# Kernel tuning notes

Hardware: AMD Instinct MI355X
Metric: run time of the kernel (lower is better)

The kernel has to match this reference:

```python
import jax, jax.numpy as jnp
from jax import lax
import numpy as np

NBITS = 3  # PartialSumLSQ bit width


def binarize(x):
    # straight-through sign (Binarize in BNN code modifies .data -> identity STE)
    return x + lax.stop_gradient(jnp.sign(x) - x)


def lsq(y, alpha):
    # LSQ quantizer for partial sums: q = round(clamp(y/a, Qn, Qp)) * a, STE round,
    # gradient-scaled step size (forward value unaffected by g).
    Qn, Qp = -(2 ** (NBITS - 1)), 2 ** (NBITS - 1) - 1
    g = 1.0 / np.sqrt(y.size * Qp)
    a = alpha * g + lax.stop_gradient(alpha - alpha * g)
    yc = jnp.clip(y / a, Qn, Qp)
    yq = yc + lax.stop_gradient(jnp.round(yc) - yc)
    return yq * a


def split_slices(xp, cgroups):
    # xp: [B, 128*cgroups, H+2, W+2]; reproduces split_tensor_128/256/512 ordering:
    # channel group outermost, then col offset j, then row offset i.
    H, W = xp.shape[2] - 2, xp.shape[3] - 2
    sl = [xp[:, g * 128:(g + 1) * 128, i:i + H, j:j + W]
          for g in range(cgroups) for j in range(3) for i in range(3)]
    return jnp.stack(sl)  # [S, B, 128, H, W]


def psum_stage(x, w, b, alpha, cgroups):
    # emulated 3x3 binary conv: pad, split into S shifted 128-ch slices, per-slice
    # binarized 1x1 conv + bias, LSQ-quantize each partial sum, accumulate.
    xp = jnp.pad(binarize(x), ((0, 0), (0, 0), (1, 1), (1, 1)))
    xs = split_slices(xp, cgroups)                      # [S,B,128,H,W]
    y = jnp.einsum('sbchw,soc->sbohw', xs, binarize(w)) + b[:, None, :, None, None]
    return jax.vmap(lsq)(y, alpha).sum(0)               # [B,Cout,H,W]


def maxpool2(x):
    return lax.reduce_window(x, -jnp.inf, lax.max, (1, 1, 2, 2), (1, 1, 2, 2), 'VALID')


def bn(x, g, b):
    # eval-mode BatchNorm with running_mean=0, running_var=1 -> affine
    s = (1, -1) + (1,) * (x.ndim - 2)
    return x * g.reshape(s) + b.reshape(s)


def htanh(x):
    return jnp.clip(x, -1.0, 1.0)


def _forward(x, conv1_w, conv1_b, s2_w, s2_b, s2_a, s3_w, s3_b, s3_a,
             s4_w, s4_b, s4_a, s5_w, s5_b, s5_a, s6_w, s6_b, s6_a,
             bn1_g, bn1_b, bn2_g, bn2_b, bn3_g, bn3_b, bn4_g, bn4_b,
             bn5_g, bn5_b, bn6_g, bn6_b, fc1_w, fc1_b, fc2_w, fc2_b,
             fc3_w, fc3_b, fbn1_g, fbn1_b, fbn2_g, fbn2_b, fbn3_g, fbn3_b):
    # conv1: 3->128 3x3 pad1; input has 3 channels -> not binarized, weight binarized
    h = lax.conv_general_dilated(x, binarize(conv1_w), (1, 1), ((1, 1), (1, 1)),
                                 dimension_numbers=('NCHW', 'OIHW', 'NCHW'))
    h = h + conv1_b[None, :, None, None]
    h = htanh(bn(h, bn1_g, bn1_b))
    h = psum_stage(h, s2_w, s2_b, s2_a, 1)   # 128->128, 9 slices, 32x32
    h = maxpool2(h)                          # 16x16
    h = htanh(bn(h, bn2_g, bn2_b))
    h = psum_stage(h, s3_w, s3_b, s3_a, 1)   # 128->256, 9 slices
    h = htanh(bn(h, bn3_g, bn3_b))
    h = psum_stage(h, s4_w, s4_b, s4_a, 2)   # 256->256, 18 slices
    h = maxpool2(h)                          # 8x8
    h = htanh(bn(h, bn4_g, bn4_b))
    h = psum_stage(h, s5_w, s5_b, s5_a, 2)   # 256->512, 18 slices
    h = htanh(bn(h, bn5_g, bn5_b))
    h = psum_stage(h, s6_w, s6_b, s6_a, 4)   # 512->512, 36 slices
    h = maxpool2(h)                          # 4x4
    h = htanh(bn(h, bn6_g, bn6_b))
    # binarized classifier: 512*4*4 -> 1024 -> 1024 -> num_classes
    f = binarize(h.reshape(h.shape[0], -1))
    f = f @ binarize(fc1_w).T + fc1_b
    f = htanh(f * fbn1_g + fbn1_b)
    f = binarize(f) @ binarize(fc2_w).T + fc2_b
    f = htanh(f * fbn2_g + fbn2_b)
    f = binarize(f) @ binarize(fc3_w).T + fc3_b
    return f * fbn3_g + fbn3_b


def setup_inputs() -> dict:
    key = jax.random.key(0)
    ks = iter(jax.random.split(key, 80))
    def rn(shape, scale=1.0):
        return jax.random.normal(next(ks), shape, jnp.float32) * scale
    d = {}
    d['x'] = rn((64, 3, 32, 32))
    d['conv1_w'] = rn((128, 3, 3, 3), 0.1)
    d['conv1_b'] = rn((128,), 0.01)
    stages = {'s2': (9, 128), 's3': (9, 256), 's4': (18, 256),
              's5': (18, 512), 's6': (36, 512)}
    for name, (S, co) in stages.items():
        d[name + '_w'] = rn((S, co, 128), 0.1)
        d[name + '_b'] = rn((S, co), 0.01)
        d[name + '_a'] = jax.random.uniform(next(ks), (S,), jnp.float32, 0.05, 0.15)
    for i, c in zip(range(1, 7), [128, 128, 256, 256, 512, 512]):
        d[f'bn{i}_g'] = jnp.ones((c,), jnp.float32) + rn((c,), 0.01)
        d[f'bn{i}_b'] = rn((c,), 0.01)
    d['fc1_w'] = rn((1024, 512 * 16), 0.02); d['fc1_b'] = rn((1024,), 0.01)
    d['fc2_w'] = rn((1024, 1024), 0.02);     d['fc2_b'] = rn((1024,), 0.01)
    d['fc3_w'] = rn((10, 1024), 0.02);       d['fc3_b'] = rn((10,), 0.01)
    for i, c in zip(range(1, 4), [1024, 1024, 10]):
        d[f'fbn{i}_g'] = jnp.ones((c,), jnp.float32) + rn((c,), 0.01)
        d[f'fbn{i}_b'] = rn((c,), 0.01)
    return d


def reference(x, conv1_w, conv1_b, s2_w, s2_b, s2_a, s3_w, s3_b, s3_a,
              s4_w, s4_b, s4_a, s5_w, s5_b, s5_a, s6_w, s6_b, s6_a,
              bn1_g, bn1_b, bn2_g, bn2_b, bn3_g, bn3_b, bn4_g, bn4_b,
              bn5_g, bn5_b, bn6_g, bn6_b, fc1_w, fc1_b, fc2_w, fc2_b,
              fc3_w, fc3_b, fbn1_g, fbn1_b, fbn2_g, fbn2_b, fbn3_g, fbn3_b):
    return _forward(x, conv1_w, conv1_b, s2_w, s2_b, s2_a, s3_w, s3_b, s3_a,
                    s4_w, s4_b, s4_a, s5_w, s5_b, s5_a, s6_w, s6_b, s6_a,
                    bn1_g, bn1_b, bn2_g, bn2_b, bn3_g, bn3_b, bn4_g, bn4_b,
                    bn5_g, bn5_b, bn6_g, bn6_b, fc1_w, fc1_b, fc2_w, fc2_b,
                    fc3_w, fc3_b, fbn1_g, fbn1_b, fbn2_g, fbn2_b, fbn3_g, fbn3_b)
```

## Files before the change

### kernel.cpp

```cpp
#include <hip/hip_runtime.h>
#include <hip/hip_bf16.h>

typedef unsigned long long u64;

struct PackArgs {
    const float* w[7];
    u64* out[7];
    int cnt[7];
    int total;
};

__global__ void k_packall(PackArgs A) {
    int gid = blockIdx.x * blockDim.x + threadIdx.x;
    int wid = gid >> 6;
    int lane = threadIdx.x & 63;
    if (wid >= A.total) return;
    int seg = 0, base = 0, pre = 0;
#pragma unroll
    for (int t = 0; t < 7; ++t) {
        if (wid >= pre) { seg = t; base = pre; }
        pre += A.cnt[t];
    }
    int li = wid - base;
    const float* p = A.w[seg] + ((size_t)li << 6);
    u64 m = __ballot(p[lane] > 0.f);
    if (lane == 0) A.out[seg][li] = m;
}

__global__ void k_packw_fc1(const float* __restrict__ w, u64* __restrict__ outT) {
    int gid = blockIdx.x * blockDim.x + threadIdx.x;
    int wid = gid >> 6;
    int lane = threadIdx.x & 63;
    if (wid >= 1024 * 8) return;
    int row = wid >> 3, gk = wid & 7;
    int g = gk >> 1, k = gk & 1;
    int c = g * 128 + k * 64 + lane;
    const float* p = w + (size_t)row * 8192 + (size_t)c * 16;
    float arr[16];
#pragma unroll
    for (int q = 0; q < 4; ++q) {
        float4 f = ((const float4*)p)[q];
        arr[4 * q + 0] = f.x; arr[4 * q + 1] = f.y;
        arr[4 * q + 2] = f.z; arr[4 * q + 3] = f.w;
    }
#pragma unroll
    for (int h = 0; h < 4; ++h)
#pragma unroll
    for (int xq = 0; xq < 4; ++xq) {
        u64 m = __ballot(arr[h * 4 + xq] > 0.f);
        if (lane == 0) {
            int wd = g * 32 + h * 8 + xq * 2 + k;
            outT[(size_t)wd * 1024 + row] = m;
        }
    }
}

struct LutArgs {
    const float* alpha[5];
    const float* bias[5];
    int off[5];
    int Cout[5];
    double ysize[5];
    int total;
};

__global__ void k_lutall(LutArgs A, double* __restrict__ lut2) {
    int idx = blockIdx.x * blockDim.x + threadIdx.x;
    if (idx >= A.total) return;
    int seg = 0;
#pragma unroll
    for (int t = 1; t < 5; ++t) if (idx >= A.off[t]) seg = t;
    int li = idx - A.off[seg];
    int s = li / A.Cout[seg];
    double gq = 1.0 / sqrt(A.ysize[seg] * 3.0);
    double al = (double)A.alpha[seg][s];
    double tg = al * gq;
    double a  = tg + (al - tg);
    double b  = (double)A.bias[seg][li];
    double q0 = rint(fmin(fmax(b / a, -4.0), 3.0));
    double qp = rint(fmin(fmax((2.0 + b) / a, -4.0), 3.0));
    double qn = rint(fmin(fmax((-2.0 + b) / a, -4.0), 3.0));
    double cz = q0 * a;
    lut2[(size_t)idx * 2 + 0] = qp * a - cz;
    lut2[(size_t)idx * 2 + 1] = qn * a - cz;
}

struct CzArgs {
    const float* alpha[5];
    const float* bias[5];
    int off[5];
    int S[5];
    int Cout[5];
    double ysize[5];
    int total;
};

__global__ void k_cz(CzArgs A, double* __restrict__ czv) {
    int idx = blockIdx.x * blockDim.x + threadIdx.x;
    if (idx >= A.total) return;
    int seg = 0;
#pragma unroll
    for (int t = 1; t < 5; ++t) if (idx >= A.off[t]) seg = t;
    int o = idx - A.off[seg];
    double gq = 1.0 / sqrt(A.ysize[seg] * 3.0);
    double CZ = 0.0;
    for (int s = 0; s < A.S[seg]; ++s) {
        double al = (double)A.alpha[seg][s];
        double tg = al * gq;
        double a  = tg + (al - tg);
        double b  = (double)A.bias[seg][s * A.Cout[seg] + o];
        double q0 = rint(fmin(fmax(b / a, -4.0), 3.0));
        CZ += q0 * a;
    }
    czv[idx] = CZ;
}

__global__ __launch_bounds__(128)
void k_conv1(const float* __restrict__ x, const float* __restrict__ w,
             const float* __restrict__ cb, const float* __restrict__ g1,
             const float* __restrict__ b1, u64* __restrict__ apack) {
    __shared__ double xs[3][3][34];
    int h = blockIdx.x & 31;
    int b = blockIdx.x >> 5;
    int tid = threadIdx.x;
    for (int idx = tid; idx < 306; idx += 128) {
        int dyy = idx / 102;
        int rem = idx - dyy * 102;
        int ci = rem / 34;
        int col = rem - ci * 34;
        int y = h + dyy - 1, xx = col - 1;
        double v = 0.0;
        if ((unsigned)y < 32u && (unsigned)xx < 32u)
            v = (double)x[((b * 3 + ci) * 32 + y) * 32 + xx];
        xs[dyy][ci][col] = v;
    }
    __syncthreads();
    int o = tid;
    double sg[3][3][3];
#pragma unroll
    for (int ci = 0; ci < 3; ++ci)
#pragma unroll
    for (int ky = 0; ky < 3; ++ky)
#pragma unroll
    for (int kx = 0; kx < 3; ++kx) {
        float wv = w[o * 27 + (ci * 3 + ky) * 3 + kx];
        sg[kx][ci][ky] = wv > 0.f ? 1.0 : (wv < 0.f ? -1.0 : 0.0);
    }
    double cbv = (double)cb[o], g1v = (double)g1[o], b1v = (double)b1[o];
    double A0 = 0.0, A1 = 0.0, A2 = 0.0;
    for (int pc = 0; pc < 34; ++pc) {
        double v[3][3];
#pragma unroll
        for (int ky = 0; ky < 3; ++ky)
#pragma unroll
        for (int ci = 0; ci < 3; ++ci)
            v[ky][ci] = xs[ky][ci][pc];
        A2 = 0.0;
#pragma unroll
        for (int ci = 0; ci < 3; ++ci)
#pragma unroll
        for (int ky = 0; ky < 3; ++ky) {
            A0 += v[ky][ci] * sg[2][ci][ky];
            A1 += v[ky][ci] * sg[1][ci][ky];
            A2 += v[ky][ci] * sg[0][ci][ky];
        }
        if (pc >= 2) {
            int wc = pc - 2;
            double t = (A0 + cbv) * g1v + b1v;
            u64 m = __ballot(t > 0.0);
            if ((tid & 63) == 0)
                apack[((size_t)(b * 1024 + h * 32 + wc)) * 2 + (tid >> 6)] = m;
        }
        A0 = A1; A1 = A2;
    }
}

template <int POOL, int G, int H, int W, int Cout, int OCHUNK, int NC>
__global__ __launch_bounds__(POOL * OCHUNK)
void k_stage(const u64* __restrict__ apack, const u64* __restrict__ wpack,
             const double* __restrict__ lut2, const double* __restrict__ czv,
             const float* __restrict__ gam, const float* __restrict__ bet,
             u64* __restrict__ opack) {
    constexpr int CW = W / NC;
    constexpr int Ho = H / POOL, Wo = W / POOL;
    constexpr int NOC = Cout / OCHUNK;
    constexpr int NROW = POOL + 2;
    constexpr int NCOL = CW + 2;
    constexpr int NT = POOL * OCHUNK;
    __shared__ alignas(16) u64 sact[G][NROW][NCOL][2];
    constexpr int PLP = (POOL == 2) ? 2 : 1;
    constexpr int PLO = (POOL == 2) ? OCHUNK : 1;
    constexpr int PLC = (POOL == 2) ? (CW / 2) : 1;
    __shared__ double pl[PLP][PLO][PLC];

    int bi = blockIdx.x;
    int oc = bi % NOC; bi /= NOC;
    int ch = bi % NC;  bi /= NC;
    int ph = bi % Ho;
    int b  = bi / Ho;
    int tid = threadIdx.x;
    int dy = tid / OCHUNK;
    int ol = tid - dy * OCHUNK;
    int o  = oc * OCHUNK + ol;
    int c0 = ch * CW;
    int ybase = ph * POOL - 1;

    constexpr int NWD = G * NROW * NCOL;
    for (int t = tid; t < NWD; t += NT) {
        int g = t / (NROW * NCOL);
        int rr = t - g * (NROW * NCOL);
        int yy = rr / NCOL;
        int xx = rr - yy * NCOL;
        int y = ybase + yy, x = c0 - 1 + xx;
        u64 v0 = 0, v1 = 0;
        if ((unsigned)y < (unsigned)H && (unsigned)x < (unsigned)W) {
            const u64* p = apack + (((size_t)((b * G + g) * H + y)) * W + x) * 2;
            v0 = p[0]; v1 = p[1];
        }
        sact[g][yy][xx][0] = v0;
        sact[g][yy][xx][1] = v1;
    }
    __syncthreads();

    double CZ = czv[o];
    double acc[CW];
#pragma unroll
    for (int c = 0; c < CW; ++c) acc[c] = CZ;

#pragma unroll
    for (int g = 0; g < G; ++g) {
#pragma unroll
        for (int j = 0; j < 3; ++j) {
#pragma unroll
            for (int i = 0; i < 3; ++i) {
                int s = g * 9 + j * 3 + i;
                int y = ph * POOL + dy + i - 1;
                if ((unsigned)y >= (unsigned)H) continue;
                size_t so = (size_t)s * Cout + o;
                u64 w0 = wpack[so * 2], w1 = wpack[so * 2 + 1];
                double dp = lut2[so * 2], dn = lut2[so * 2 + 1];
                bool cutlo = (ch == 0) && (j == 0);
                bool cuthi = (ch == NC - 1) && (j == 2);
                int yy = dy + i;
#pragma unroll
                for (int c = 0; c < CW; ++c) {
                    if ((c == 0 && cutlo) || (c == CW - 1 && cuthi)) continue;
                    u64 a0 = sact[g][yy][c + j][0];
                    u64 a1 = sact[g][yy][c + j][1];
                    int d = __popcll(a0 ^ w0) + __popcll(a1 ^ w1);
                    double val = (d < 64) ? dp : dn;
                    val = (d == 64) ? 0.0 : val;
                    acc[c] += val;
                }
            }
        }
    }

    double gv = (double)gam[o], bv = (double)bet[o];
    if constexpr (POOL == 1) {
#pragma unroll
        for (int c = 0; c < CW; ++c) {
            double t = acc[c] * gv + bv;
            u64 bm = __ballot(t > 0.0);
            if ((tid & 63) == 0) {
                int pw = c0 + c;
                opack[(((size_t)(b * (Cout >> 7) + (o >> 7)) * Ho + ph) * Wo + pw) * 2
                      + ((o >> 6) & 1)] = bm;
            }
        }
    } else {
#pragma unroll
        for (int c2 = 0; c2 < CW / 2; ++c2)
            pl[dy][ol][c2] = fmax(acc[2 * c2], acc[2 * c2 + 1]);
        __syncthreads();
        if (dy == 0) {
#pragma unroll
            for (int c2 = 0; c2 < CW / 2; ++c2) {
                double m = fmax(pl[0][ol][c2], pl[1][ol][c2]);
                double t = m * gv + bv;
                u64 bm = __ballot(t > 0.0);
                if ((tid & 63) == 0) {
                    int pw = c0 / 2 + c2;
                    opack[(((size_t)(b * (Cout >> 7) + (o >> 7)) * Ho + ph) * Wo + pw) * 2
                          + ((o >> 6) & 1)] = bm;
                }
            }
        }
    }
}

__global__ void k_fc_pack(const u64* __restrict__ apack, const u64* __restrict__ wpack,
                          int rstride, int wstride,
                          const float* __restrict__ bias, const float* __restrict__ gam,
                          const float* __restrict__ bet, u64* __restrict__ opack,
                          int nw, int Rwords) {
    int wg = blockIdx.x % Rwords;
    int b = blockIdx.x / Rwords;
    int r = wg * 64 + threadIdx.x;
    const u64* a = apack + (size_t)b * nw;
    const u64* wp = wpack + (size_t)r * rstride;
    int d = 0;
    for (int i = 0; i < nw; ++i) d += __popcll(a[i] ^ wp[(size_t)i * wstride]);
    double isum = (double)(nw * 64 - 2 * d);
    double t = (isum + (double)bias[r]) * (double)gam[r] + (double)bet[r];
    u64 m = __ballot(t > 0.0);
    if (threadIdx.x == 0) opack[(size_t)b * Rwords + wg] = m;
}

__global__ void k_fc3(const u64* __restrict__ apack, const u64* __restrict__ wpack,
                      const float* __restrict__ bias, const float* __restrict__ gam,
                      const float* __restrict__ bet, float* __restrict__ out) {
    int idx = blockIdx.x * blockDim.x + threadIdx.x;
    if (idx >= 640) return;
    int b = idx / 10, r = idx % 10;
    const u64* a = apack + (size_t)b * 16;
    const u64* wp = wpack + (size_t)r * 16;
    int d = 0;
    for (int i = 0; i < 16; ++i) d += __popcll(a[i] ^ wp[i]);
    double isum = (double)(1024 - 2 * d);
    out[idx] = (float)((isum + (double)bias[r]) * (double)gam[r] + (double)bet[r]);
}


extern "C" void kernel_launch(void* const* d_in, const int* in_sizes, int n_in,
                              void* d_out, int out_size, void* d_ws, size_t ws_size,
                              hipStream_t stream) {
    const float* x       = (const float*)d_in[0];
    const float* conv1_w = (const float*)d_in[1];
    const float* conv1_b = (const float*)d_in[2];
    const float* s_w[5]  = {(const float*)d_in[3], (const float*)d_in[6], (const float*)d_in[9],
                            (const float*)d_in[12], (const float*)d_in[15]};
    const float* s_b[5]  = {(const float*)d_in[4], (const float*)d_in[7], (const float*)d_in[10],
                            (const float*)d_in[13], (const float*)d_in[16]};
    const float* s_a[5]  = {(const float*)d_in[5], (const float*)d_in[8], (const float*)d_in[11],
                            (const float*)d_in[14], (const float*)d_in[17]};
    const float* bn_g[6], *bn_b[6];
    for (int i = 0; i < 6; ++i) { bn_g[i] = (const float*)d_in[18 + 2 * i]; bn_b[i] = (const float*)d_in[19 + 2 * i]; }
    const float* fc1_w = (const float*)d_in[30]; const float* fc1_b = (const float*)d_in[31];
    const float* fc2_w = (const float*)d_in[32]; const float* fc2_b = (const float*)d_in[33];
    const float* fc3_w = (const float*)d_in[34]; const float* fc3_b = (const float*)d_in[35];
    const float* fbn_g[3], *fbn_b[3];
    for (int i = 0; i < 3; ++i) { fbn_g[i] = (const float*)d_in[36 + 2 * i]; fbn_b[i] = (const float*)d_in[37 + 2 * i]; }

    size_t off = 0;
    auto alloc = [&](size_t bytes) { off = (off + 255) & ~(size_t)255; size_t o = off; off += bytes; return o; };
    char* ws = (char*)d_ws;
    size_t o_apA = alloc(1048576);
    size_t o_apB = alloc(1048576);
    size_t o_wp  = alloc((size_t)71424 * 8);
    size_t o_lut = alloc((size_t)35712 * 2 * 8);
    size_t o_cz  = alloc((size_t)1664 * 8);
    size_t o_wf1 = alloc((size_t)1024 * 128 * 8);
    size_t o_wf2 = alloc((size_t)1024 * 16 * 8);
    size_t o_wf3 = alloc((size_t)10 * 16 * 8 + 256);
    size_t o_fp1 = alloc((size_t)64 * 16 * 8);
    size_t o_fp2 = alloc((size_t)64 * 16 * 8);
    if (off > ws_size) return;

    u64* apA = (u64*)(ws + o_apA);
    u64* apB = (u64*)(ws + o_apB);
    u64* wpbuf = (u64*)(ws + o_wp);
    double* lut2 = (double*)(ws + o_lut);
    double* czbuf = (double*)(ws + o_cz);
    u64* wf1T = (u64*)(ws + o_wf1);
    u64* wf2 = (u64*)(ws + o_wf2);
    u64* wf3 = (u64*)(ws + o_wf3);
    u64* fp1 = (u64*)(ws + o_fp1);
    u64* fp2 = (u64*)(ws + o_fp2);

    const int rowoff[5] = {0, 1152, 3456, 8064, 17280};
    const int czoff[5]  = {0, 128, 384, 640, 1152};
    u64* wp[5];  double* lt[5];  double* cz[5];
    for (int i = 0; i < 5; ++i) {
        wp[i] = wpbuf + (size_t)rowoff[i] * 2;
        lt[i] = lut2 + (size_t)rowoff[i] * 2;
        cz[i] = czbuf + czoff[i];
    }

    PackArgs PA;
    const int scnt[5] = {2304, 4608, 9216, 18432, 36864};
    int tot = 0;
    for (int i = 0; i < 5; ++i) { PA.w[i] = s_w[i]; PA.out[i] = wp[i]; PA.cnt[i] = scnt[i]; tot += scnt[i]; }
    PA.w[5] = fc2_w; PA.out[5] = wf2; PA.cnt[5] = 1024 * 16; tot += 1024 * 16;
    PA.w[6] = fc3_w; PA.out[6] = wf3; PA.cnt[6] = 160;       tot += 160;
    PA.total = tot;
    {
        long long thr = (long long)tot * 64;
        k_packall<<<(int)((thr + 255) / 256), 256, 0, stream>>>(PA);
    }
    k_packw_fc1<<<(1024 * 8 * 64) / 256, 256, 0, stream>>>(fc1_w, wf1T);

    LutArgs LA;
    const int sS[5]    = {9, 9, 18, 18, 36};
    const int sCout[5] = {128, 256, 256, 512, 512};
    const double sYsz[5] = {8388608.0, 4194304.0, 4194304.0, 2097152.0, 2097152.0};
    for (int i = 0; i < 5; ++i) {
        LA.alpha[i] = s_a[i]; LA.bias[i] = s_b[i];
        LA.off[i] = rowoff[i]; LA.Cout[i] = sCout[i]; LA.ysize[i] = sYsz[i];
    }
    LA.total = 35712;
    k_lutall<<<(35712 + 255) / 256, 256, 0, stream>>>(LA, lut2);

    CzArgs CA;
    for (int i = 0; i < 5; ++i) {
        CA.alpha[i] = s_a[i]; CA.bias[i] = s_b[i];
        CA.off[i] = czoff[i]; CA.S[i] = sS[i]; CA.Cout[i] = sCout[i]; CA.ysize[i] = sYsz[i];
    }
    CA.total = 1664;
    k_cz<<<(1664 + 255) / 256, 256, 0, stream>>>(CA, czbuf);

    k_conv1<<<64 * 32, 128, 0, stream>>>(x, conv1_w, conv1_b, bn_g[0], bn_b[0], apA);

    k_stage<2, 1, 32, 32, 128, 128, 2><<<64 * 16 * 2, 256, 0, stream>>>(
        apA, wp[0], lt[0], cz[0], bn_g[1], bn_b[1], apB);
    k_stage<1, 1, 16, 16, 256, 256, 2><<<64 * 16 * 2, 256, 0, stream>>>(
        apB, wp[1], lt[1], cz[1], bn_g[2], bn_b[2], apA);
    k_stage<2, 2, 16, 16, 256, 256, 2><<<64 * 8 * 2, 512, 0, stream>>>(
        apA, wp[2], lt[2], cz[2], bn_g[3], bn_b[3], apB);
    k_stage<1, 2, 8, 8, 512, 512, 2><<<64 * 8 * 2, 512, 0, stream>>>(
        apB, wp[3], lt[3], cz[3], bn_g[4], bn_b[4], apA);
    k_stage<2, 4, 8, 8, 512, 256, 2><<<64 * 4 * 2 * 2, 512, 0, stream>>>(
        apA, wp[4], lt[4], cz[4], bn_g[5], bn_b[5], apB);

    k_fc_pack<<<64 * 16, 64, 0, stream>>>(apB, wf1T, 1, 1024, fc1_b, fbn_g[0], fbn_b[0], fp1, 128, 16);
    k_fc_pack<<<64 * 16, 64, 0, stream>>>(fp1, wf2, 16, 1, fc2_b, fbn_g[1], fbn_b[1], fp2, 16, 16);
    k_fc3<<<10, 64, 0, stream>>>(fp2, wf3, fc3_b, fbn_g[2], fbn_b[2], (float*)d_out);
}
```

Measured before the change: 237.3 us.

## Fuse prep and FC kernels, interleave weight/LUT, and restructure stage tiling for in-register pooling

Merges the four weight-packing and LUT/cz precompute kernels into one k_prep launch and the three FC kernels into a single per-batch k_fc_all kernel that keeps intermediate bits in shared memory. Interleaves packed weights with their two LUT doubles in one 4-word record so each slice needs one contiguous load. Reworks k_stage so each thread owns all pooling rows and several output columns, which lets max-pooling happen in registers without the shared pool buffer and extra barrier, and changes per-stage grid/thread shapes. This cuts launch count and sync overhead but raises register pressure per thread, and the FC kernel runs only 64 blocks.

```diff
diff --git a/kernel.cpp b/kernel.cpp
--- a/kernel.cpp
+++ b/kernel.cpp
@@ -1,118 +1,108 @@
 #include <hip/hip_runtime.h>
 #include <hip/hip_bf16.h>
+#include <math.h>
 
 typedef unsigned long long u64;
 
-struct PackArgs {
+struct PrepArgs {
     const float* w[7];
     u64* out[7];
     int cnt[7];
-    int total;
-};
-
-__global__ void k_packall(PackArgs A) {
-    int gid = blockIdx.x * blockDim.x + threadIdx.x;
-    int wid = gid >> 6;
-    int lane = threadIdx.x & 63;
-    if (wid >= A.total) return;
-    int seg = 0, base = 0, pre = 0;
-#pragma unroll
-    for (int t = 0; t < 7; ++t) {
-        if (wid >= pre) { seg = t; base = pre; }
-        pre += A.cnt[t];
-    }
-    int li = wid - base;
-    const float* p = A.w[seg] + ((size_t)li << 6);
-    u64 m = __ballot(p[lane] > 0.f);
-    if (lane == 0) A.out[seg][li] = m;
-}
-
-__global__ void k_packw_fc1(const float* __restrict__ w, u64* __restrict__ outT) {
-    int gid = blockIdx.x * blockDim.x + threadIdx.x;
-    int wid = gid >> 6;
-    int lane = threadIdx.x & 63;
-    if (wid >= 1024 * 8) return;
-    int row = wid >> 3, gk = wid & 7;
-    int g = gk >> 1, k = gk & 1;
-    int c = g * 128 + k * 64 + lane;
-    const float* p = w + (size_t)row * 8192 + (size_t)c * 16;
-    float arr[16];
-#pragma unroll
-    for (int q = 0; q < 4; ++q) {
-        float4 f = ((const float4*)p)[q];
-        arr[4 * q + 0] = f.x; arr[4 * q + 1] = f.y;
-        arr[4 * q + 2] = f.z; arr[4 * q + 3] = f.w;
-    }
-#pragma unroll
-    for (int h = 0; h < 4; ++h)
-#pragma unroll
-    for (int xq = 0; xq < 4; ++xq) {
-        u64 m = __ballot(arr[h * 4 + xq] > 0.f);
-        if (lane == 0) {
-            int wd = g * 32 + h * 8 + xq * 2 + k;
-            outT[(size_t)wd * 1024 + row] = m;
-        }
-    }
-}
-
-struct LutArgs {
+    int mode[7];
+    const float* fc1w;
+    u64* fc1T;
     const float* alpha[5];
     const float* bias[5];
-    int off[5];
-    int Cout[5];
-    double ysize[5];
-    int total;
+    int loff[5];
+    int lCout[5];
+    double gq[5];
+    u64* wlut;
+    double* czv;
+    int czoff[5];
+    int czS[5];
+    int R1, R2, R3, R4;
 };
 
-__global__ void k_lutall(LutArgs A, double* __restrict__ lut2) {
-    int idx = blockIdx.x * blockDim.x + threadIdx.x;
-    if (idx >= A.total) return;
-    int seg = 0;
-#pragma unroll
-    for (int t = 1; t < 5; ++t) if (idx >= A.off[t]) seg = t;
-    int li = idx - A.off[seg];
-    int s = li / A.Cout[seg];
-    double gq = 1.0 / sqrt(A.ysize[seg] * 3.0);
-    double al = (double)A.alpha[seg][s];
-    double tg = al * gq;
-    double a  = tg + (al - tg);
-    double b  = (double)A.bias[seg][li];
-    double q0 = rint(fmin(fmax(b / a, -4.0), 3.0));
-    double qp = rint(fmin(fmax((2.0 + b) / a, -4.0), 3.0));
-    double qn = rint(fmin(fmax((-2.0 + b) / a, -4.0), 3.0));
-    double cz = q0 * a;
-    lut2[(size_t)idx * 2 + 0] = qp * a - cz;
-    lut2[(size_t)idx * 2 + 1] = qn * a - cz;
-}
-
-struct CzArgs {
-    const float* alpha[5];
-    const float* bias[5];
-    int off[5];
-    int S[5];
-    int Cout[5];
-    double ysize[5];
-    int total;
-};
-
-__global__ void k_cz(CzArgs A, double* __restrict__ czv) {
-    int idx = blockIdx.x * blockDim.x + threadIdx.x;
-    if (idx >= A.total) return;
-    int seg = 0;
-#pragma unroll
-    for (int t = 1; t < 5; ++t) if (idx >= A.off[t]) seg = t;
-    int o = idx - A.off[seg];
-    double gq = 1.0 / sqrt(A.ysize[seg] * 3.0);
-    double CZ = 0.0;
-    for (int s = 0; s < A.S[seg]; ++s) {
+__global__ __launch_bounds__(256)
+void k_prep(PrepArgs A) {
+    int gid = blockIdx.x * 256 + threadIdx.x;
+    int lane = threadIdx.x & 63;
+    if (gid < A.R1) {
+        int wid = gid >> 6;
+        int seg = 0, base = 0, pre = 0;
+#pragma unroll
+        for (int t = 0; t < 7; ++t) {
+            if (wid >= pre) { seg = t; base = pre; }
+            pre += A.cnt[t];
+        }
+        int li = wid - base;
+        const float* p = A.w[seg] + ((size_t)li << 6);
+        u64 m = __ballot(p[lane] > 0.f);
+        if (lane == 0) {
+            int mode = A.mode[seg];
+            size_t idx = (mode == 1) ? ((size_t)(li >> 1) * 4 + (li & 1))
+                       : (mode == 2) ? ((size_t)(li & 15) * 1024 + (li >> 4))
+                       : (size_t)li;
+            A.out[seg][idx] = m;
+        }
+    } else if (gid < A.R2) {
+        int wid = (gid - A.R1) >> 6;
+        int row = wid >> 3, gk = wid & 7;
+        int g = gk >> 1, k = gk & 1;
+        int c = g * 128 + k * 64 + lane;
+        const float* p = A.fc1w + (size_t)row * 8192 + (size_t)c * 16;
+        float arr[16];
+#pragma unroll
+        for (int q = 0; q < 4; ++q) {
+            float4 f = ((const float4*)p)[q];
+            arr[4 * q + 0] = f.x; arr[4 * q + 1] = f.y;
+            arr[4 * q + 2] = f.z; arr[4 * q + 3] = f.w;
+        }
+#pragma unroll
+        for (int h = 0; h < 4; ++h)
+#pragma unroll
+        for (int xq = 0; xq < 4; ++xq) {
+            u64 m = __ballot(arr[h * 4 + xq] > 0.f);
+            if (lane == 0) {
+                int wd = g * 32 + h * 8 + xq * 2 + k;
+                A.fc1T[(size_t)wd * 1024 + row] = m;
+            }
+        }
+    } else if (gid < A.R3) {
+        int idx = gid - A.R2;
+        int seg = 0;
+#pragma unroll
+        for (int t = 1; t < 5; ++t) if (idx >= A.loff[t]) seg = t;
+        int li = idx - A.loff[seg];
+        int s = li / A.lCout[seg];
         double al = (double)A.alpha[seg][s];
-        double tg = al * gq;
+        double tg = al * A.gq[seg];
         double a  = tg + (al - tg);
-        double b  = (double)A.bias[seg][s * A.Cout[seg] + o];
+        double b  = (double)A.bias[seg][li];
         double q0 = rint(fmin(fmax(b / a, -4.0), 3.0));
-        CZ += q0 * a;
-    }
-    czv[idx] = CZ;
+        double qp = rint(fmin(fmax((2.0 + b) / a, -4.0), 3.0));
+        double qn = rint(fmin(fmax((-2.0 + b) / a, -4.0), 3.0));
+        double cz = q0 * a;
+        A.wlut[(size_t)idx * 4 + 2] = __double_as_longlong(qp * a - cz);
+        A.wlut[(size_t)idx * 4 + 3] = __double_as_longlong(qn * a - cz);
+    } else if (gid < A.R4) {
+        int idx = gid - A.R3;
+        int seg = 0;
+#pragma unroll
+        for (int t = 1; t < 5; ++t) if (idx >= A.czoff[t]) seg = t;
+        int o = idx - A.czoff[seg];
+        int Cout = A.lCout[seg];
+        double CZ = 0.0;
+        for (int s = 0; s < A.czS[seg]; ++s) {
+            double al = (double)A.alpha[seg][s];
+            double tg = al * A.gq[seg];
+            double a  = tg + (al - tg);
+            double b  = (double)A.bias[seg][s * Cout + o];
+            double q0 = rint(fmin(fmax(b / a, -4.0), 3.0));
+            CZ += q0 * a;
+        }
+        A.czv[idx] = CZ;
+    }
 }
 
 __global__ __launch_bounds__(128)
@@ -175,43 +165,40 @@
     }
 }
 
-template <int POOL, int G, int H, int W, int Cout, int OCHUNK, int NC>
-__global__ __launch_bounds__(POOL * OCHUNK)
-void k_stage(const u64* __restrict__ apack, const u64* __restrict__ wpack,
-             const double* __restrict__ lut2, const double* __restrict__ czv,
+template <int POOL, int G, int H, int W, int Cout, int OCH, int NCH, int CWP>
+__global__ __launch_bounds__(NCH * OCH)
+void k_stage(const u64* __restrict__ apack, const u64* __restrict__ wlut,
+             const double* __restrict__ czv,
              const float* __restrict__ gam, const float* __restrict__ bet,
              u64* __restrict__ opack) {
-    constexpr int CW = W / NC;
     constexpr int Ho = H / POOL, Wo = W / POOL;
-    constexpr int NOC = Cout / OCHUNK;
+    constexpr int NOC = Cout / OCH;
+    constexpr int CRAW = NCH * CWP * POOL;
     constexpr int NROW = POOL + 2;
-    constexpr int NCOL = CW + 2;
-    constexpr int NT = POOL * OCHUNK;
+    constexpr int NCOL = CRAW + 2;
+    constexpr int NT = NCH * OCH;
+    constexpr int CB = Wo / (NCH * CWP);
     __shared__ alignas(16) u64 sact[G][NROW][NCOL][2];
-    constexpr int PLP = (POOL == 2) ? 2 : 1;
-    constexpr int PLO = (POOL == 2) ? OCHUNK : 1;
-    constexpr int PLC = (POOL == 2) ? (CW / 2) : 1;
-    __shared__ double pl[PLP][PLO][PLC];
 
     int bi = blockIdx.x;
     int oc = bi % NOC; bi /= NOC;
-    int ch = bi % NC;  bi /= NC;
+    int cb = bi % CB;  bi /= CB;
     int ph = bi % Ho;
     int b  = bi / Ho;
     int tid = threadIdx.x;
-    int dy = tid / OCHUNK;
-    int ol = tid - dy * OCHUNK;
-    int o  = oc * OCHUNK + ol;
-    int c0 = ch * CW;
+    int ch = tid / OCH;
+    int ol = tid - ch * OCH;
+    int o  = oc * OCH + ol;
+    int colb = cb * CRAW;
+    int c0 = colb + ch * CWP * POOL;
     int ybase = ph * POOL - 1;
 
-    constexpr int NWD = G * NROW * NCOL;
-    for (int t = tid; t < NWD; t += NT) {
+    for (int t = tid; t < G * NROW * NCOL; t += NT) {
         int g = t / (NROW * NCOL);
         int rr = t - g * (NROW * NCOL);
         int yy = rr / NCOL;
         int xx = rr - yy * NCOL;
-        int y = ybase + yy, x = c0 - 1 + xx;
+        int y = ybase + yy, x = colb - 1 + xx;
         u64 v0 = 0, v1 = 0;
         if ((unsigned)y < (unsigned)H && (unsigned)x < (unsigned)W) {
             const u64* p = apack + (((size_t)((b * G + g) * H + y)) * W + x) * 2;
@@ -223,9 +210,12 @@
     __syncthreads();
 
     double CZ = czv[o];
-    double acc[CW];
-#pragma unroll
-    for (int c = 0; c < CW; ++c) acc[c] = CZ;
+    double acc[CWP * POOL * POOL];
+#pragma unroll
+    for (int k = 0; k < CWP * POOL * POOL; ++k) acc[k] = CZ;
+
+    const bool lo0 = (c0 == 0);
+    const bool hiW = (c0 + CWP * POOL == W);
 
 #pragma unroll
     for (int g = 0; g < G; ++g) {
@@ -233,92 +223,102 @@
         for (int j = 0; j < 3; ++j) {
 #pragma unroll
             for (int i = 0; i < 3; ++i) {
-                int s = g * 9 + j * 3 + i;
-                int y = ph * POOL + dy + i - 1;
-                if ((unsigned)y >= (unsigned)H) continue;
+                const int s = g * 9 + j * 3 + i;
                 size_t so = (size_t)s * Cout + o;
-                u64 w0 = wpack[so * 2], w1 = wpack[so * 2 + 1];
-                double dp = lut2[so * 2], dn = lut2[so * 2 + 1];
-                bool cutlo = (ch == 0) && (j == 0);
-                bool cuthi = (ch == NC - 1) && (j == 2);
-                int yy = dy + i;
-#pragma unroll
-                for (int c = 0; c < CW; ++c) {
-                    if ((c == 0 && cutlo) || (c == CW - 1 && cuthi)) continue;
-                    u64 a0 = sact[g][yy][c + j][0];
-                    u64 a1 = sact[g][yy][c + j][1];
-                    int d = __popcll(a0 ^ w0) + __popcll(a1 ^ w1);
-                    double val = (d < 64) ? dp : dn;
-                    val = (d == 64) ? 0.0 : val;
-                    acc[c] += val;
+                const u64* wl = wlut + so * 4;
+                u64 w0 = wl[0], w1 = wl[1];
+                double dp = __longlong_as_double(wl[2]);
+                double dn = __longlong_as_double(wl[3]);
+#pragma unroll
+                for (int dy = 0; dy < POOL; ++dy) {
+                    int y = ph * POOL + dy + i - 1;
+                    if ((unsigned)y >= (unsigned)H) continue;
+                    const int yy = dy + i;
+#pragma unroll
+                    for (int cc = 0; cc < CWP * POOL; ++cc) {
+                        if (cc == 0 && j == 0 && lo0) continue;
+                        if (cc == CWP * POOL - 1 && j == 2 && hiW) continue;
+                        int xx = ch * CWP * POOL + cc + j;
+                        u64 a0 = sact[g][yy][xx][0];
+                        u64 a1 = sact[g][yy][xx][1];
+                        int d = __popcll(a0 ^ w0) + __popcll(a1 ^ w1);
+                        double val = (d < 64) ? dp : dn;
+                        val = (d == 64) ? 0.0 : val;
+                        acc[cc * POOL + dy] += val;
+                    }
                 }
             }
         }
     }
 
     double gv = (double)gam[o], bv = (double)bet[o];
-    if constexpr (POOL == 1) {
-#pragma unroll
-        for (int c = 0; c < CW; ++c) {
-            double t = acc[c] * gv + bv;
-            u64 bm = __ballot(t > 0.0);
-            if ((tid & 63) == 0) {
-                int pw = c0 + c;
-                opack[(((size_t)(b * (Cout >> 7) + (o >> 7)) * Ho + ph) * Wo + pw) * 2
-                      + ((o >> 6) & 1)] = bm;
-            }
-        }
-    } else {
-#pragma unroll
-        for (int c2 = 0; c2 < CW / 2; ++c2)
-            pl[dy][ol][c2] = fmax(acc[2 * c2], acc[2 * c2 + 1]);
-        __syncthreads();
-        if (dy == 0) {
-#pragma unroll
-            for (int c2 = 0; c2 < CW / 2; ++c2) {
-                double m = fmax(pl[0][ol][c2], pl[1][ol][c2]);
-                double t = m * gv + bv;
-                u64 bm = __ballot(t > 0.0);
-                if ((tid & 63) == 0) {
-                    int pw = c0 / 2 + c2;
-                    opack[(((size_t)(b * (Cout >> 7) + (o >> 7)) * Ho + ph) * Wo + pw) * 2
-                          + ((o >> 6) & 1)] = bm;
-                }
-            }
+#pragma unroll
+    for (int cw = 0; cw < CWP; ++cw) {
+        double m;
+        if constexpr (POOL == 1) {
+            m = acc[cw];
+        } else {
+            m = fmax(fmax(acc[(cw * 2 + 0) * 2 + 0], acc[(cw * 2 + 0) * 2 + 1]),
+                     fmax(acc[(cw * 2 + 1) * 2 + 0], acc[(cw * 2 + 1) * 2 + 1]));
+        }
+        double tt = m * gv + bv;
+        u64 bm = __ballot(tt > 0.0);
+        if ((tid & 63) == 0) {
+            int pw = c0 / POOL + cw;
+            opack[(((size_t)(b * (Cout >> 7) + (o >> 7)) * Ho + ph) * Wo + pw) * 2
+                  + ((o >> 6) & 1)] = bm;
         }
     }
 }
 
-__global__ void k_fc_pack(const u64* __restrict__ apack, const u64* __restrict__ wpack,
-                          int rstride, int wstride,
-                          const float* __restrict__ bias, const float* __restrict__ gam,
-                          const float* __restrict__ bet, u64* __restrict__ opack,
-                          int nw, int Rwords) {
-    int wg = blockIdx.x % Rwords;
-    int b = blockIdx.x / Rwords;
-    int r = wg * 64 + threadIdx.x;
-    const u64* a = apack + (size_t)b * nw;
-    const u64* wp = wpack + (size_t)r * rstride;
-    int d = 0;
-    for (int i = 0; i < nw; ++i) d += __popcll(a[i] ^ wp[(size_t)i * wstride]);
-    double isum = (double)(nw * 64 - 2 * d);
-    double t = (isum + (double)bias[r]) * (double)gam[r] + (double)bet[r];
-    u64 m = __ballot(t > 0.0);
-    if (threadIdx.x == 0) opack[(size_t)b * Rwords + wg] = m;
-}
-
-__global__ void k_fc3(const u64* __restrict__ apack, const u64* __restrict__ wpack,
-                      const float* __restrict__ bias, const float* __restrict__ gam,
-                      const float* __restrict__ bet, float* __restrict__ out) {
-    int idx = blockIdx.x * blockDim.x + threadIdx.x;
-    if (idx >= 640) return;
-    int b = idx / 10, r = idx % 10;
-    const u64* a = apack + (size_t)b * 16;
-    const u64* wp = wpack + (size_t)r * 16;
-    int d = 0;
-    for (int i = 0; i < 16; ++i) d += __popcll(a[i] ^ wp[i]);
-    double isum = (double)(1024 - 2 * d);
-    out[idx] = (float)((isum + (double)bias[r]) * (double)gam[r] + (double)bet[r]);
+__global__ __launch_bounds__(1024)
+void k_fc_all(const u64* __restrict__ abits, const u64* __restrict__ wf1T,
+              const float* __restrict__ b1, const float* __restrict__ g1,
+              const float* __restrict__ a1,
+              const u64* __restrict__ wf2T,
+              const float* __restrict__ b2, const float* __restrict__ g2,
+              const float* __restrict__ a2,
+              const u64* __restrict__ wf3,
+              const float* __restrict__ b3, const float* __restrict__ g3,
+              const float* __restrict__ a3,
+              float* __restrict__ out) {
+    __shared__ u64 sa[128];
+    __shared__ u64 sp1[16];
+    __shared__ u64 sp2[16];
+    int b = blockIdx.x;
+    int t = threadIdx.x;
+    if (t < 128) sa[t] = abits[(size_t)b * 128 + t];
+    __syncthreads();
+    {
+        int d = 0;
+#pragma unroll 16
+        for (int i = 0; i < 128; ++i)
+            d += __popcll(sa[i] ^ wf1T[(size_t)i * 1024 + t]);
+        double isum = (double)(8192 - 2 * d);
+        double v = (isum + (double)b1[t]) * (double)g1[t] + (double)a1[t];
+        u64 m = __ballot(v > 0.0);
+        if ((t & 63) == 0) sp1[t >> 6] = m;
+    }
+    __syncthreads();
+    {
+        int d = 0;
+#pragma unroll
+        for (int i = 0; i < 16; ++i)
+            d += __popcll(sp1[i] ^ wf2T[(size_t)i * 1024 + t]);
+        double isum = (double)(1024 - 2 * d);
+        double v = (isum + (double)b2[t]) * (double)g2[t] + (double)a2[t];
+        u64 m = __ballot(v > 0.0);
+        if ((t & 63) == 0) sp2[t >> 6] = m;
+    }
+    __syncthreads();
+    if (t < 10) {
+        int d = 0;
+#pragma unroll
+        for (int i = 0; i < 16; ++i)
+            d += __popcll(sp2[i] ^ wf3[t * 16 + i]);
+        double isum = (double)(1024 - 2 * d);
+        out[b * 10 + t] = (float)((isum + (double)b3[t]) * (double)g3[t] + (double)a3[t]);
+    }
 }
 
 
@@ -345,84 +345,70 @@
     size_t off = 0;
     auto alloc = [&](size_t bytes) { off = (off + 255) & ~(size_t)255; size_t o = off; off += bytes; return o; };
     char* ws = (char*)d_ws;
-    size_t o_apA = alloc(1048576);
-    size_t o_apB = alloc(1048576);
-    size_t o_wp  = alloc((size_t)71424 * 8);
-    size_t o_lut = alloc((size_t)35712 * 2 * 8);
-    size_t o_cz  = alloc((size_t)1664 * 8);
-    size_t o_wf1 = alloc((size_t)1024 * 128 * 8);
-    size_t o_wf2 = alloc((size_t)1024 * 16 * 8);
-    size_t o_wf3 = alloc((size_t)10 * 16 * 8 + 256);
-    size_t o_fp1 = alloc((size_t)64 * 16 * 8);
-    size_t o_fp2 = alloc((size_t)64 * 16 * 8);
+    size_t o_apA  = alloc(1048576);
+    size_t o_apB  = alloc(1048576);
+    size_t o_wlut = alloc((size_t)35712 * 4 * 8);
+    size_t o_cz   = alloc((size_t)1664 * 8);
+    size_t o_wf1  = alloc((size_t)1024 * 128 * 8);
+    size_t o_wf2  = alloc((size_t)1024 * 16 * 8);
+    size_t o_wf3  = alloc((size_t)160 * 8);
     if (off > ws_size) return;
 
     u64* apA = (u64*)(ws + o_apA);
     u64* apB = (u64*)(ws + o_apB);
-    u64* wpbuf = (u64*)(ws + o_wp);
-    double* lut2 = (double*)(ws + o_lut);
+    u64* wlut = (u64*)(ws + o_wlut);
     double* czbuf = (double*)(ws + o_cz);
     u64* wf1T = (u64*)(ws + o_wf1);
-    u64* wf2 = (u64*)(ws + o_wf2);
+    u64* wf2T = (u64*)(ws + o_wf2);
     u64* wf3 = (u64*)(ws + o_wf3);
-    u64* fp1 = (u64*)(ws + o_fp1);
-    u64* fp2 = (u64*)(ws + o_fp2);
 
     const int rowoff[5] = {0, 1152, 3456, 8064, 17280};
     const int czoff[5]  = {0, 128, 384, 640, 1152};
-    u64* wp[5];  double* lt[5];  double* cz[5];
+    const int sS[5]     = {9, 9, 18, 18, 36};
+    const int sCout[5]  = {128, 256, 256, 512, 512};
+    const double sYsz[5] = {8388608.0, 4194304.0, 4194304.0, 2097152.0, 2097152.0};
+
+    PrepArgs PA;
+    const int scnt[5] = {2304, 4608, 9216, 18432, 36864};
+    int totw = 0;
     for (int i = 0; i < 5; ++i) {
-        wp[i] = wpbuf + (size_t)rowoff[i] * 2;
-        lt[i] = lut2 + (size_t)rowoff[i] * 2;
-        cz[i] = czbuf + czoff[i];
-    }
-
-    PackArgs PA;
-    const int scnt[5] = {2304, 4608, 9216, 18432, 36864};
-    int tot = 0;
-    for (int i = 0; i < 5; ++i) { PA.w[i] = s_w[i]; PA.out[i] = wp[i]; PA.cnt[i] = scnt[i]; tot += scnt[i]; }
-    PA.w[5] = fc2_w; PA.out[5] = wf2; PA.cnt[5] = 1024 * 16; tot += 1024 * 16;
-    PA.w[6] = fc3_w; PA.out[6] = wf3; PA.cnt[6] = 160;       tot += 160;
-    PA.total = tot;
-    {
-        long long thr = (long long)tot * 64;
-        k_packall<<<(int)((thr + 255) / 256), 256, 0, stream>>>(PA);
-    }
-    k_packw_fc1<<<(1024 * 8 * 64) / 256, 256, 0, stream>>>(fc1_w, wf1T);
-
-    LutArgs LA;
-    const int sS[5]    = {9, 9, 18, 18, 36};
-    const int sCout[5] = {128, 256, 256, 512, 512};
-    const double sYsz[5] = {8388608.0, 4194304.0, 4194304.0, 2097152.0, 2097152.0};
+        PA.w[i] = s_w[i];
+        PA.out[i] = wlut + (size_t)rowoff[i] * 4;
+        PA.cnt[i] = scnt[i];
+        PA.mode[i] = 1;
+        totw += scnt[i];
+    }
+    PA.w[5] = fc2_w; PA.out[5] = wf2T; PA.cnt[5] = 1024 * 16; PA.mode[5] = 2; totw += 1024 * 16;
+    PA.w[6] = fc3_w; PA.out[6] = wf3;  PA.cnt[6] = 160;       PA.mode[6] = 0; totw += 160;
+    PA.fc1w = fc1_w; PA.fc1T = wf1T;
     for (int i = 0; i < 5; ++i) {
-        LA.alpha[i] = s_a[i]; LA.bias[i] = s_b[i];
-        LA.off[i] = rowoff[i]; LA.Cout[i] = sCout[i]; LA.ysize[i] = sYsz[i];
-    }
-    LA.total = 35712;
-    k_lutall<<<(35712 + 255) / 256, 256, 0, stream>>>(LA, lut2);
-
-    CzArgs CA;
-    for (int i = 0; i < 5; ++i) {
-        CA.alpha[i] = s_a[i]; CA.bias[i] = s_b[i];
-        CA.off[i] = czoff[i]; CA.S[i] = sS[i]; CA.Cout[i] = sCout[i]; CA.ysize[i] = sYsz[i];
-    }
-    CA.total = 1664;
-    k_cz<<<(1664 + 255) / 256, 256, 0, stream>>>(CA, czbuf);
+        PA.alpha[i] = s_a[i]; PA.bias[i] = s_b[i];
+        PA.loff[i] = rowoff[i]; PA.lCout[i] = sCout[i];
+        PA.gq[i] = 1.0 / sqrt(sYsz[i] * 3.0);
+        PA.czoff[i] = czoff[i]; PA.czS[i] = sS[i];
+    }
+    PA.wlut = wlut; PA.czv = czbuf;
+    PA.R1 = totw * 64;
+    PA.R2 = PA.R1 + 1024 * 8 * 64;
+    PA.R3 = PA.R2 + 35712;
+    PA.R4 = PA.R3 + 1664;
+    k_prep<<<(PA.R4 + 255) / 256, 256, 0, stream>>>(PA);
 
     k_conv1<<<64 * 32, 128, 0, stream>>>(x, conv1_w, conv1_b, bn_g[0], bn_b[0], apA);
 
-    k_stage<2, 1, 32, 32, 128, 128, 2><<<64 * 16 * 2, 256, 0, stream>>>(
-        apA, wp[0], lt[0], cz[0], bn_g[1], bn_b[1], apB);
-    k_stage<1, 1, 16, 16, 256, 256, 2><<<64 * 16 * 2, 256, 0, stream>>>(
-        apB, wp[1], lt[1], cz[1], bn_g[2], bn_b[2], apA);
-    k_stage<2, 2, 16, 16, 256, 256, 2><<<64 * 8 * 2, 512, 0, stream>>>(
-        apA, wp[2], lt[2], cz[2], bn_g[3], bn_b[3], apB);
-    k_stage<1, 2, 8, 8, 512, 512, 2><<<64 * 8 * 2, 512, 0, stream>>>(
-        apB, wp[3], lt[3], cz[3], bn_g[4], bn_b[4], apA);
-    k_stage<2, 4, 8, 8, 512, 256, 2><<<64 * 4 * 2 * 2, 512, 0, stream>>>(
-        apA, wp[4], lt[4], cz[4], bn_g[5], bn_b[5], apB);
-
-    k_fc_pack<<<64 * 16, 64, 0, stream>>>(apB, wf1T, 1, 1024, fc1_b, fbn_g[0], fbn_b[0], fp1, 128, 16);
-    k_fc_pack<<<64 * 16, 64, 0, stream>>>(fp1, wf2, 16, 1, fc2_b, fbn_g[1], fbn_b[1], fp2, 16, 16);
-    k_fc3<<<10, 64, 0, stream>>>(fp2, wf3, fc3_b, fbn_g[2], fbn_b[2], (float*)d_out);
+    k_stage<2, 1, 32, 32, 128, 128, 2, 2><<<64 * 16 * 4 * 1, 256, 0, stream>>>(
+        apA, wlut + (size_t)rowoff[0] * 4, czbuf + czoff[0], bn_g[1], bn_b[1], apB);
+    k_stage<1, 1, 16, 16, 256, 256, 1, 8><<<64 * 16 * 2 * 1, 256, 0, stream>>>(
+        apB, wlut + (size_t)rowoff[1] * 4, czbuf + czoff[1], bn_g[2], bn_b[2], apA);
+    k_stage<2, 2, 16, 16, 256, 256, 1, 2><<<64 * 8 * 4 * 1, 256, 0, stream>>>(
+        apA, wlut + (size_t)rowoff[2] * 4, czbuf + czoff[2], bn_g[3], bn_b[3], apB);
+    k_stage<1, 2, 8, 8, 512, 256, 1, 4><<<64 * 8 * 2 * 2, 256, 0, stream>>>(
+        apB, wlut + (size_t)rowoff[3] * 4, czbuf + czoff[3], bn_g[4], bn_b[4], apA);
+    k_stage<2, 4, 8, 8, 512, 256, 1, 1><<<64 * 4 * 4 * 2, 256, 0, stream>>>(
+        apA, wlut + (size_t)rowoff[4] * 4, czbuf + czoff[4], bn_g[5], bn_b[5], apB);
+
+    k_fc_all<<<64, 1024, 0, stream>>>(apB, wf1T, fc1_b, fbn_g[0], fbn_b[0],
+                                      wf2T, fc2_b, fbn_g[1], fbn_b[1],
+                                      wf3, fc3_b, fbn_g[2], fbn_b[2],
+                                      (float*)d_out);
 }
```

Measured after the change: 221.9 us. 1.07x faster.
